# Kernel tuning notes

Measured on AMD Instinct MI355X. Metric: run time of the kernel, lower is better.

## Reference

```python
import jax, jax.numpy as jnp
import numpy as np

B, N, K, E, H, V = 128, 256, 4, 300, 150, 32000  # batch, nodes/tree, max children, embed, hidden, vocab
DELTA = 1.0


def setup_inputs() -> dict:
    key = jax.random.key(0)
    ks = jax.random.split(key, 8)
    query = jax.random.randint(ks[0], (B, N), 0, V, dtype=jnp.int32)
    pos = jax.random.randint(ks[1], (B, N), 0, V, dtype=jnp.int32)
    neg = jax.random.randint(ks[2], (B, N), 0, V, dtype=jnp.int32)
    # Complete K-ary tree over N nodes: children of node t are {K*t+1, ..., K*t+K} < N; root = node 0.
    ch = np.full((N, K), -1, dtype=np.int32)
    for t in range(N):
        for j in range(K):
            c = K * t + 1 + j
            if c < N:
                ch[t, j] = c
    children = jnp.asarray(ch)
    emb = jax.random.normal(ks[3], (V, E), dtype=jnp.float32) * 0.02
    W_iou = jax.random.normal(ks[4], (E, 3 * H), dtype=jnp.float32) * 0.05
    U_iou = jax.random.normal(ks[5], (H, 3 * H), dtype=jnp.float32) * 0.05
    b_iou = jnp.zeros((3 * H,), jnp.float32)
    W_f = jax.random.normal(ks[6], (E, H), dtype=jnp.float32) * 0.05
    U_f = jax.random.normal(ks[7], (H, H), dtype=jnp.float32) * 0.05
    b_f = jnp.zeros((H,), jnp.float32)
    return {"query": query, "pos": pos, "neg": neg, "children": children,
            "emb": emb, "W_iou": W_iou, "U_iou": U_iou, "b_iou": b_iou,
            "W_f": W_f, "U_f": U_f, "b_f": b_f}


def _childsum_treelstm(x, children, W_iou, U_iou, b_iou, W_f, U_f, b_f):
    """x: [B, N, E] node embeddings. Returns root (c, h): each [B, H]."""
    Bn, Nn, _ = x.shape
    Hh = U_f.shape[0]
    h0 = jnp.zeros((Bn, Nn, Hh), x.dtype)
    c0 = jnp.zeros((Bn, Nn, Hh), x.dtype)

    def step(carry, t):
        h_all, c_all = carry
        ch = children[t]                        # [K] child indices, -1 = padding
        mask = (ch >= 0)
        idx = jnp.where(mask, ch, 0)
        m = mask.astype(x.dtype)[None, :, None]  # [1, K, 1]
        h_k = h_all[:, idx] * m                 # [B, K, H]
        c_k = c_all[:, idx] * m
        h_sum = h_k.sum(axis=1)                 # child-sum h_tilde [B, H]
        x_t = x[:, t]                           # [B, E]
        iou = x_t @ W_iou + h_sum @ U_iou + b_iou
        i, o, u = jnp.split(iou, 3, axis=-1)
        i = jax.nn.sigmoid(i)
        o = jax.nn.sigmoid(o)
        u = jnp.tanh(u)
        # per-child forget gates: f_jk = sigmoid(W_f x_j + U_f h_k + b_f)
        f = jax.nn.sigmoid((x_t @ W_f + b_f)[:, None, :] + h_k @ U_f)  # [B, K, H]
        c_t = i * u + (f * c_k).sum(axis=1)     # c_k already masked
        h_t = o * jnp.tanh(c_t)
        return (h_all.at[:, t].set(h_t), c_all.at[:, t].set(c_t)), None

    # children have larger indices than parents -> process N-1 .. 0 (root last)
    (h_all, c_all), _ = jax.lax.scan(step, (h0, c0), jnp.arange(Nn - 1, -1, -1))
    return c_all[:, 0], h_all[:, 0]


def _cosine(a, b):
    num = (a * b).sum(-1)
    den = jnp.sqrt((a * a).sum(-1) * (b * b).sum(-1)) + 1e-8
    return num / den


def reference(query, pos, neg, children, emb, W_iou, U_iou, b_iou, W_f, U_f, b_f):
    qc, _ = _childsum_treelstm(emb[query], children, W_iou, U_iou, b_iou, W_f, U_f, b_f)
    pc, _ = _childsum_treelstm(emb[pos], children, W_iou, U_iou, b_iou, W_f, U_f, b_f)
    nc, _ = _childsum_treelstm(emb[neg], children, W_iou, U_iou, b_iou, W_f, U_f, b_f)
    a = _cosine(qc, pc)  # [B]
    b = _cosine(qc, nc)  # [B]
    return jax.nn.relu(DELTA - a + b)
```

## Files before the change

### kernel.cpp

```cpp
#include <hip/hip_runtime.h>
#include <hip/hip_bf16.h>

typedef short short8 __attribute__((ext_vector_type(8)));
typedef float floatx4 __attribute__((ext_vector_type(4)));
typedef unsigned short ushort;

#define Bb 128
#define Nn 256
#define Hh 150
#define HK 160
#define Vv 32000
#define NROW 384
#define PROJC 600
#define NINT 64
#define ZROW (Vv + NROW * NINT)

#define WTN 640

__device__ __forceinline__ float sigf(float x) { return 1.0f / (1.0f + __expf(-x)); }
__device__ __forceinline__ float tanhf_(float x) { return 1.0f - 2.0f / (__expf(2.0f * x) + 1.0f); }
__device__ __forceinline__ float bf2f(ushort s) { union { float f; unsigned u; } v; v.u = ((unsigned)s) << 16; return v.f; }
__device__ __forceinline__ ushort f2bf(float f) { __hip_bfloat16 h = __float2bfloat16(f); return *(ushort*)&h; }

__global__ __launch_bounds__(256) void k_prep(
    const float* __restrict__ W_iou, const float* __restrict__ W_f,
    const float* __restrict__ U_iou, const float* __restrict__ U_f,
    const float* __restrict__ b_iou, const float* __restrict__ b_f,
    short* __restrict__ Wt, short* __restrict__ Uti, short* __restrict__ Utf,
    float* __restrict__ biasw, ushort* __restrict__ h_u, float* __restrict__ c_u)
{
    int idx = blockIdx.x * 256 + threadIdx.x;
    const int nWt = 320 * WTN, nUi = 160 * 464, nUf = 160 * 160;
    if (idx < nWt) {
        int k = idx / WTN, n = idx % WTN;
        float v = 0.f;
        if (k < 300) { if (n < 450) v = W_iou[k * 450 + n]; else if (n < 600) v = W_f[k * 150 + (n - 450)]; }
        Wt[n * 320 + k] = (short)f2bf(v);
    } else if (idx < nWt + nUi) {
        int i2 = idx - nWt; int k = i2 / 464, n = i2 % 464;
        float v = (k < 150 && n < 450) ? U_iou[k * 450 + n] : 0.f;
        Uti[n * 160 + k] = (short)f2bf(v);
    } else if (idx < nWt + nUi + nUf) {
        int i2 = idx - nWt - nUi; int k = i2 / 160, n = i2 % 160;
        float v = (k < 150 && n < 150) ? U_f[k * 150 + n] : 0.f;
        Utf[n * 160 + k] = (short)f2bf(v);
    } else if (idx < nWt + nUi + nUf + WTN) {
        int n = idx - nWt - nUi - nUf;
        biasw[n] = n < 450 ? b_iou[n] : (n < 600 ? b_f[n - 450] : 0.f);
    } else if (idx < nWt + nUi + nUf + WTN + HK) {
        int k = idx - (nWt + nUi + nUf + WTN);
        h_u[(long)ZROW * HK + k] = 0;
        c_u[(long)ZROW * HK + k] = 0.f;
    }
}

__global__ __launch_bounds__(256) void k_vproj(
    const float* __restrict__ emb, const short* __restrict__ Wt,
    const float* __restrict__ biasw, ushort* __restrict__ proj)
{
    __shared__ __align__(16) short As[2][32][328];
    const int tid = threadIdx.x;

    const int bid = blockIdx.x;
    const int xcd = bid & 7, li = bid >> 3;
    const int wgid = xcd * 125 + li;

    const int cg = wgid % 5;
    const int rg = wgid / 5;
    const int rowbase = rg * 160;

    const int w = tid >> 6, lane = tid & 63;
    const int m = lane & 15, kq = (lane >> 4) * 8;
    const int t0 = cg * 8 + w * 2;
    const int col0 = t0 * 16 + m;
    const int col1 = col0 + 16;

    short8 bq0[10], bq1[10];
    #pragma unroll
    for (int ks = 0; ks < 10; ks++) {
        bq0[ks] = *(const short8*)(Wt + (long)col0 * 320 + kq + ks * 32);
        bq1[ks] = *(const short8*)(Wt + (long)col1 * 320 + kq + ks * 32);
    }
    const float bias0 = biasw[col0];
    const float bias1 = biasw[col1];

    for (int i = tid; i < 2 * 32 * 5; i += 256) {
        int bz = i / 160, r2 = (i % 160) / 5, kk = (i % 5) * 4;
        *(short4*)&As[bz][r2][300 + kk] = make_short4(0, 0, 0, 0);
    }

    {
        const float4* src = (const float4*)emb + (long)rowbase * 75;
        for (int i = tid; i < 2400; i += 256) {
            int r = i / 75, k0 = (i % 75) * 4;
            float4 x = src[i];
            short4 sv;
            sv.x = (short)f2bf(x.x); sv.y = (short)f2bf(x.y);
            sv.z = (short)f2bf(x.z); sv.w = (short)f2bf(x.w);
            *(short4*)&As[0][r][k0] = sv;
        }
    }
    __syncthreads();

    for (int c = 0; c < 5; c++) {
        const int buf = c & 1;

        float4 x[10];
        if (c < 4) {
            const float4* src = (const float4*)emb + (long)(rowbase + (c + 1) * 32) * 75;
            #pragma unroll
            for (int j = 0; j < 10; j++) {
                int i = tid + j * 256;
                if (i < 2400) x[j] = src[i];
            }
        }

        floatx4 a00 = {0.f,0.f,0.f,0.f}, a01 = a00, a10 = a00, a11 = a00;
        #pragma unroll
        for (int ks = 0; ks < 10; ks++) {
            short8 a0 = *(const short8*)&As[buf][m][kq + ks * 32];
            short8 a1 = *(const short8*)&As[buf][16 + m][kq + ks * 32];
            a00 = __builtin_amdgcn_mfma_f32_16x16x32_bf16(a0, bq0[ks], a00, 0, 0, 0);
            a01 = __builtin_amdgcn_mfma_f32_16x16x32_bf16(a0, bq1[ks], a01, 0, 0, 0);
            a10 = __builtin_amdgcn_mfma_f32_16x16x32_bf16(a1, bq0[ks], a10, 0, 0, 0);
            a11 = __builtin_amdgcn_mfma_f32_16x16x32_bf16(a1, bq1[ks], a11, 0, 0, 0);
        }

        {
            int v0 = rowbase + c * 32;
            int rb = (lane >> 4) * 4;
            if (col0 < PROJC) {
                #pragma unroll
                for (int reg = 0; reg < 4; reg++) {
                    proj[(long)(v0 + rb + reg) * PROJC + col0]      = f2bf(a00[reg] + bias0);
                    proj[(long)(v0 + 16 + rb + reg) * PROJC + col0] = f2bf(a10[reg] + bias0);
                }
            }
            if (col1 < PROJC) {
                #pragma unroll
                for (int reg = 0; reg < 4; reg++) {
                    proj[(long)(v0 + rb + reg) * PROJC + col1]      = f2bf(a01[reg] + bias1);
                    proj[(long)(v0 + 16 + rb + reg) * PROJC + col1] = f2bf(a11[reg] + bias1);
                }
            }
        }

        if (c < 4) {
            #pragma unroll
            for (int j = 0; j < 10; j++) {
                int i = tid + j * 256;
                if (i < 2400) {
                    int r = i / 75, k0 = (i % 75) * 4;
                    short4 sv;
                    sv.x = (short)f2bf(x[j].x); sv.y = (short)f2bf(x[j].y);
                    sv.z = (short)f2bf(x[j].z); sv.w = (short)f2bf(x[j].w);
                    *(short4*)&As[buf ^ 1][r][k0] = sv;
                }
            }
        }
        __syncthreads();
    }
}

__global__ __launch_bounds__(256) void k_vleaf(
    const ushort* __restrict__ proj, ushort* __restrict__ h_u, float* __restrict__ c_u)
{
    int idx = blockIdx.x * 256 + threadIdx.x;
    int v = idx / 20, k0 = (idx % 20) * 8;
    const ushort* pr = proj + (long)v * PROJC;
    ushort hv[8]; float cvv[8];
    #pragma unroll
    for (int e = 0; e < 8; e++) {
        int k = k0 + e;
        if (k < Hh) {
            float iv = sigf(bf2f(pr[k]));
            float ov = sigf(bf2f(pr[150 + k]));
            float uv = tanhf_(bf2f(pr[300 + k]));
            float cc = iv * uv;
            cvv[e] = cc;
            hv[e] = f2bf(ov * tanhf_(cc));
        } else { cvv[e] = 0.f; hv[e] = 0; }
    }
    *(int4*)(h_u + (long)v * HK + k0) = *(int4*)hv;
    *(float4*)(c_u + (long)v * HK + k0)     = make_float4(cvv[0], cvv[1], cvv[2], cvv[3]);
    *(float4*)(c_u + (long)v * HK + k0 + 4) = make_float4(cvv[4], cvv[5], cvv[6], cvv[7]);
}

__global__ __launch_bounds__(256) void k_level(
    int t_base, int t_cnt,
    const int* __restrict__ tq, const int* __restrict__ tp, const int* __restrict__ tn,
    const int* __restrict__ children, const ushort* __restrict__ proj,
    const short* __restrict__ Uti, const short* __restrict__ Utf,
    ushort* __restrict__ h_u, float* __restrict__ c_u)
{
    __shared__ __align__(16) short As[2][5][16][168];
    __shared__ int idx_s[2][16][4];
    __shared__ int tok_s[2][16];

    const int tid = threadIdx.x;
    const int chunk = blockIdx.x / 24;
    const int r0 = (blockIdx.x % 24) * 16;
    const int tA = t_base + chunk * 2;
    const int nT = min(2, t_base + t_cnt - tA);

    if (tid < 64 * nT) {
        int tt = tid >> 6, q = tid & 63;
        int r = q >> 2, j = q & 3;
        int t = tA + tt;
        int rg = r0 + r, g = rg >> 7, b = rg & 127;
        const int* tok = (g == 0) ? tq : (g == 1 ? tp : tn);
        int ch = children[t * 4 + j];
        int idx;
        if (ch < 0)        idx = ZROW;
        else if (ch >= 64) idx = tok[b * Nn + ch];
        else               idx = Vv + rg * NINT + ch;
        idx_s[tt][r][j] = idx;
        if (j == 0) tok_s[tt][r] = tok[b * Nn + t];
    }
    __syncthreads();

    for (int i = tid; i < 320 * nT; i += 256) {
        int tt = i / 320, i2 = i % 320;
        int r = i2 / 20, k0 = (i2 % 20) * 8;
        int4 v0 = *(const int4*)(h_u + (long)idx_s[tt][r][0] * HK + k0);
        int4 v1 = *(const int4*)(h_u + (long)idx_s[tt][r][1] * HK + k0);
        int4 v2 = *(const int4*)(h_u + (long)idx_s[tt][r][2] * HK + k0);
        int4 v3 = *(const int4*)(h_u + (long)idx_s[tt][r][3] * HK + k0);
        *(int4*)&As[tt][1][r][k0] = v0;
        *(int4*)&As[tt][2][r][k0] = v1;
        *(int4*)&As[tt][3][r][k0] = v2;
        *(int4*)&As[tt][4][r][k0] = v3;
        ushort s[8];
        const ushort* p0 = (const ushort*)&v0; const ushort* p1 = (const ushort*)&v1;
        const ushort* p2 = (const ushort*)&v2; const ushort* p3 = (const ushort*)&v3;
        #pragma unroll
        for (int e = 0; e < 8; e++)
            s[e] = f2bf(bf2f(p0[e]) + bf2f(p1[e]) + bf2f(p2[e]) + bf2f(p3[e]));
        *(int4*)&As[tt][0][r][k0] = *(int4*)s;
    }
    __syncthreads();

    const int w = tid >> 6, lane = tid & 63;
    const int m = lane & 15, kq = (lane >> 4) * 8;
    const int rbase = (lane >> 4) * 4;

    for (int nt = w; nt < 10; nt += 4) {
        int col = nt * 16 + m;

        short8 Bi[5], Bo[5], Bu[5], Bf[5];
        #pragma unroll
        for (int ks = 0; ks < 5; ks++) {
            Bi[ks] = *(const short8*)(Uti + (long)(col)       * HK + kq + ks * 32);
            Bo[ks] = *(const short8*)(Uti + (long)(150 + col) * HK + kq + ks * 32);
            Bu[ks] = *(const short8*)(Uti + (long)(300 + col) * HK + kq + ks * 32);
            Bf[ks] = *(const short8*)(Utf + (long)(col)       * HK + kq + ks * 32);
        }

        for (int tt = 0; tt < nT; ++tt) {
            int t = tA + tt;

            float pv0[4], pv1[4], pv2[4], pv3[4];
            float cu0[4], cu1[4], cu2[4], cu3[4];
            if (col < Hh) {
                #pragma unroll
                for (int reg = 0; reg < 4; reg++) {
                    const ushort* pr = proj + (long)tok_s[tt][rbase + reg] * PROJC;
                    pv0[reg] = bf2f(pr[col]);
                    pv1[reg] = bf2f(pr[150 + col]);
                    pv2[reg] = bf2f(pr[300 + col]);
                    pv3[reg] = bf2f(pr[450 + col]);
                    cu0[reg] = c_u[(long)idx_s[tt][rbase + reg][0] * HK + col];
                    cu1[reg] = c_u[(long)idx_s[tt][rbase + reg][1] * HK + col];
                    cu2[reg] = c_u[(long)idx_s[tt][rbase + reg][2] * HK + col];
                    cu3[reg] = c_u[(long)idx_s[tt][rbase + reg][3] * HK + col];
                }
            }

            floatx4 ai = {0.f,0.f,0.f,0.f}, ao = ai, au = ai;
            floatx4 af0 = ai, af1 = ai, af2 = ai, af3 = ai;
            #pragma unroll
            for (int ks = 0; ks < 5; ks++) {
                short8 asum = *(const short8*)&As[tt][0][m][kq + ks * 32];
                short8 ac0  = *(const short8*)&As[tt][1][m][kq + ks * 32];
                short8 ac1  = *(const short8*)&As[tt][2][m][kq + ks * 32];
                short8 ac2  = *(const short8*)&As[tt][3][m][kq + ks * 32];
                short8 ac3  = *(const short8*)&As[tt][4][m][kq + ks * 32];
                ai  = __builtin_amdgcn_mfma_f32_16x16x32_bf16(asum, Bi[ks], ai, 0, 0, 0);
                ao  = __builtin_amdgcn_mfma_f32_16x16x32_bf16(asum, Bo[ks], ao, 0, 0, 0);
                au  = __builtin_amdgcn_mfma_f32_16x16x32_bf16(asum, Bu[ks], au, 0, 0, 0);
                af0 = __builtin_amdgcn_mfma_f32_16x16x32_bf16(ac0,  Bf[ks], af0, 0, 0, 0);
                af1 = __builtin_amdgcn_mfma_f32_16x16x32_bf16(ac1,  Bf[ks], af1, 0, 0, 0);
                af2 = __builtin_amdgcn_mfma_f32_16x16x32_bf16(ac2,  Bf[ks], af2, 0, 0, 0);
                af3 = __builtin_amdgcn_mfma_f32_16x16x32_bf16(ac3,  Bf[ks], af3, 0, 0, 0);
            }

            if (col < Hh) {
                #pragma unroll
                for (int reg = 0; reg < 4; reg++) {
                    int rg = r0 + rbase + reg;
                    float iv = sigf(pv0[reg] + ai[reg]);
                    float ov = sigf(pv1[reg] + ao[reg]);
                    float uv = tanhf_(pv2[reg] + au[reg]);
                    float fpre = pv3[reg];
                    float cv = iv * uv;
                    cv = fmaf(sigf(fpre + af0[reg]), cu0[reg], cv);
                    cv = fmaf(sigf(fpre + af1[reg]), cu1[reg], cv);
                    cv = fmaf(sigf(fpre + af2[reg]), cu2[reg], cv);
                    cv = fmaf(sigf(fpre + af3[reg]), cu3[reg], cv);
                    long o = (long)(Vv + rg * NINT + t) * HK + col;
                    c_u[o] = cv;
                    h_u[o] = f2bf(ov * tanhf_(cv));
                }
            } else {
                #pragma unroll
                for (int reg = 0; reg < 4; reg++) {
                    long o = (long)(Vv + (r0 + rbase + reg) * NINT + t) * HK + col;
                    c_u[o] = 0.f; h_u[o] = 0;
                }
            }
        }
    }
}

__global__ __launch_bounds__(64) void k_cos(const float* __restrict__ c_u, float* __restrict__ out)
{
    int b = blockIdx.x, tid = threadIdx.x;
    const float* qc = c_u + (long)(Vv + (0 * Bb + b) * NINT) * HK;
    const float* pc = c_u + (long)(Vv + (1 * Bb + b) * NINT) * HK;
    const float* nc = c_u + (long)(Vv + (2 * Bb + b) * NINT) * HK;
    float qp = 0, qn = 0, qq = 0, pp = 0, nn2 = 0;
    for (int k = tid; k < Hh; k += 64) {
        float qv = qc[k], pv = pc[k], nv = nc[k];
        qp += qv * pv; qn += qv * nv; qq += qv * qv; pp += pv * pv; nn2 += nv * nv;
    }
    #pragma unroll
    for (int off = 32; off > 0; off >>= 1) {
        qp += __shfl_down(qp, off, 64);
        qn += __shfl_down(qn, off, 64);
        qq += __shfl_down(qq, off, 64);
        pp += __shfl_down(pp, off, 64);
        nn2 += __shfl_down(nn2, off, 64);
    }
    if (tid == 0) {
        float a = qp / (sqrtf(qq * pp) + 1e-8f);
        float d = qn / (sqrtf(qq * nn2) + 1e-8f);
        out[b] = fmaxf(0.0f, 1.0f - a + d);
    }
}

extern "C" void kernel_launch(void* const* d_in, const int* in_sizes, int n_in,
                              void* d_out, int out_size, void* d_ws, size_t ws_size,
                              hipStream_t stream)
{
    const int*   tq       = (const int*)d_in[0];
    const int*   tp       = (const int*)d_in[1];
    const int*   tn       = (const int*)d_in[2];
    const int*   children = (const int*)d_in[3];
    const float* emb      = (const float*)d_in[4];
    const float* W_iou    = (const float*)d_in[5];
    const float* U_iou    = (const float*)d_in[6];
    const float* b_iou    = (const float*)d_in[7];
    const float* W_f      = (const float*)d_in[8];
    const float* U_f      = (const float*)d_in[9];
    const float* b_f      = (const float*)d_in[10];
    float* out = (float*)d_out;

    char* ws = (char*)d_ws;
    ushort* proj  = (ushort*)ws;
    ushort* h_u   = (ushort*)(ws + 38400000);
    float*  c_u   = (float*)(ws + 56504640);
    short*  Wt    = (short*)(ws + 92713920);
    short*  Uti   = (short*)(ws + 93123520);
    short*  Utf   = (short*)(ws + 93272000);
    float*  biasw = (float*)(ws + 93323200);

    k_prep<<<1194, 256, 0, stream>>>(W_iou, W_f, U_iou, U_f, b_iou, b_f,
                                     Wt, Uti, Utf, biasw, h_u, c_u);
    k_vproj<<<1000, 256, 0, stream>>>(emb, Wt, biasw, proj);
    k_vleaf<<<2500, 256, 0, stream>>>(proj, h_u, c_u);
    k_level<<<22 * 24, 256, 0, stream>>>(21, 43, tq, tp, tn, children, proj, Uti, Utf, h_u, c_u);
    k_level<<<8 * 24, 256, 0, stream>>>(5, 16, tq, tp, tn, children, proj, Uti, Utf, h_u, c_u);
    k_level<<<2 * 24, 256, 0, stream>>>(1, 4,  tq, tp, tn, children, proj, Uti, Utf, h_u, c_u);
    k_level<<<1 * 24, 256, 0, stream>>>(0, 1,  tq, tp, tn, children, proj, Uti, Utf, h_u, c_u);
    k_cos<<<Bb, 64, 0, stream>>>(c_u, out);
}
```

Baseline: 249.7 us.

## Fuse last two tree levels into one kernel and double vproj rows per block

The final two level launches (nodes 1-4 and root) become a single kernel that runs three level steps in sequence with block barriers between them. This is valid because each block owns the same 16 rows across levels. The vocab projection kernel now has each workgroup process 320 rows over 10 chunks with half the blocks, giving a new XCD remap. Child and token indices in shared memory are narrowed to ushort. The fused kernel saves one launch and its tail, but the doubled vproj work per block lowers parallelism, and ushort indices could overflow for ZROW-range values.

```diff
diff --git a/kernel.cpp b/kernel.cpp
--- a/kernel.cpp
+++ b/kernel.cpp
@@ -63,11 +63,11 @@
 
     const int bid = blockIdx.x;
     const int xcd = bid & 7, li = bid >> 3;
-    const int wgid = xcd * 125 + li;
+    const int wgid = (xcd < 4 ? xcd * 63 : 252 + (xcd - 4) * 62) + li;
 
     const int cg = wgid % 5;
     const int rg = wgid / 5;
-    const int rowbase = rg * 160;
+    const int rowbase = rg * 320;
 
     const int w = tid >> 6, lane = tid & 63;
     const int m = lane & 15, kq = (lane >> 4) * 8;
@@ -102,11 +102,11 @@
     }
     __syncthreads();
 
-    for (int c = 0; c < 5; c++) {
+    for (int c = 0; c < 10; c++) {
         const int buf = c & 1;
 
         float4 x[10];
-        if (c < 4) {
+        if (c < 9) {
             const float4* src = (const float4*)emb + (long)(rowbase + (c + 1) * 32) * 75;
             #pragma unroll
             for (int j = 0; j < 10; j++) {
@@ -145,7 +145,7 @@
             }
         }
 
-        if (c < 4) {
+        if (c < 9) {
             #pragma unroll
             for (int j = 0; j < 10; j++) {
                 int i = tid + j * 256;
@@ -186,22 +186,16 @@
     *(float4*)(c_u + (long)v * HK + k0 + 4) = make_float4(cvv[4], cvv[5], cvv[6], cvv[7]);
 }
 
-__global__ __launch_bounds__(256) void k_level(
-    int t_base, int t_cnt,
+__device__ __forceinline__ void level_step(
+    int tA, int nT, int r0,
     const int* __restrict__ tq, const int* __restrict__ tp, const int* __restrict__ tn,
     const int* __restrict__ children, const ushort* __restrict__ proj,
     const short* __restrict__ Uti, const short* __restrict__ Utf,
-    ushort* __restrict__ h_u, float* __restrict__ c_u)
-{
-    __shared__ __align__(16) short As[2][5][16][168];
-    __shared__ int idx_s[2][16][4];
-    __shared__ int tok_s[2][16];
-
+    ushort* __restrict__ h_u, float* __restrict__ c_u,
+    short (*As)[16][168] ,
+    ushort (*idx_s)[16][4], ushort (*tok_s)[16])
+{
     const int tid = threadIdx.x;
-    const int chunk = blockIdx.x / 24;
-    const int r0 = (blockIdx.x % 24) * 16;
-    const int tA = t_base + chunk * 2;
-    const int nT = min(2, t_base + t_cnt - tA);
 
     if (tid < 64 * nT) {
         int tt = tid >> 6, q = tid & 63;
@@ -214,8 +208,8 @@
         if (ch < 0)        idx = ZROW;
         else if (ch >= 64) idx = tok[b * Nn + ch];
         else               idx = Vv + rg * NINT + ch;
-        idx_s[tt][r][j] = idx;
-        if (j == 0) tok_s[tt][r] = tok[b * Nn + t];
+        idx_s[tt][r][j] = (ushort)idx;
+        if (j == 0) tok_s[tt][r] = (ushort)tok[b * Nn + t];
     }
     __syncthreads();
 
@@ -226,17 +220,17 @@
         int4 v1 = *(const int4*)(h_u + (long)idx_s[tt][r][1] * HK + k0);
         int4 v2 = *(const int4*)(h_u + (long)idx_s[tt][r][2] * HK + k0);
         int4 v3 = *(const int4*)(h_u + (long)idx_s[tt][r][3] * HK + k0);
-        *(int4*)&As[tt][1][r][k0] = v0;
-        *(int4*)&As[tt][2][r][k0] = v1;
-        *(int4*)&As[tt][3][r][k0] = v2;
-        *(int4*)&As[tt][4][r][k0] = v3;
+        *(int4*)&As[tt * 5 + 1][r][k0] = v0;
+        *(int4*)&As[tt * 5 + 2][r][k0] = v1;
+        *(int4*)&As[tt * 5 + 3][r][k0] = v2;
+        *(int4*)&As[tt * 5 + 4][r][k0] = v3;
         ushort s[8];
         const ushort* p0 = (const ushort*)&v0; const ushort* p1 = (const ushort*)&v1;
         const ushort* p2 = (const ushort*)&v2; const ushort* p3 = (const ushort*)&v3;
         #pragma unroll
         for (int e = 0; e < 8; e++)
             s[e] = f2bf(bf2f(p0[e]) + bf2f(p1[e]) + bf2f(p2[e]) + bf2f(p3[e]));
-        *(int4*)&As[tt][0][r][k0] = *(int4*)s;
+        *(int4*)&As[tt * 5 + 0][r][k0] = *(int4*)s;
     }
     __syncthreads();
 
@@ -280,11 +274,11 @@
             floatx4 af0 = ai, af1 = ai, af2 = ai, af3 = ai;
             #pragma unroll
             for (int ks = 0; ks < 5; ks++) {
-                short8 asum = *(const short8*)&As[tt][0][m][kq + ks * 32];
-                short8 ac0  = *(const short8*)&As[tt][1][m][kq + ks * 32];
-                short8 ac1  = *(const short8*)&As[tt][2][m][kq + ks * 32];
-                short8 ac2  = *(const short8*)&As[tt][3][m][kq + ks * 32];
-                short8 ac3  = *(const short8*)&As[tt][4][m][kq + ks * 32];
+                short8 asum = *(const short8*)&As[tt * 5 + 0][m][kq + ks * 32];
+                short8 ac0  = *(const short8*)&As[tt * 5 + 1][m][kq + ks * 32];
+                short8 ac1  = *(const short8*)&As[tt * 5 + 2][m][kq + ks * 32];
+                short8 ac2  = *(const short8*)&As[tt * 5 + 3][m][kq + ks * 32];
+                short8 ac3  = *(const short8*)&As[tt * 5 + 4][m][kq + ks * 32];
                 ai  = __builtin_amdgcn_mfma_f32_16x16x32_bf16(asum, Bi[ks], ai, 0, 0, 0);
                 ao  = __builtin_amdgcn_mfma_f32_16x16x32_bf16(asum, Bo[ks], ao, 0, 0, 0);
                 au  = __builtin_amdgcn_mfma_f32_16x16x32_bf16(asum, Bu[ks], au, 0, 0, 0);
@@ -322,6 +316,48 @@
     }
 }
 
+__global__ __launch_bounds__(256) void k_level(
+    int t_base, int t_cnt,
+    const int* __restrict__ tq, const int* __restrict__ tp, const int* __restrict__ tn,
+    const int* __restrict__ children, const ushort* __restrict__ proj,
+    const short* __restrict__ Uti, const short* __restrict__ Utf,
+    ushort* __restrict__ h_u, float* __restrict__ c_u)
+{
+    __shared__ __align__(16) short As[10][16][168];
+    __shared__ ushort idx_s[2][16][4];
+    __shared__ ushort tok_s[2][16];
+
+    const int chunk = blockIdx.x / 24;
+    const int r0 = (blockIdx.x % 24) * 16;
+    const int tA = t_base + chunk * 2;
+    const int nT = min(2, t_base + t_cnt - tA);
+
+    level_step(tA, nT, r0, tq, tp, tn, children, proj, Uti, Utf, h_u, c_u,
+               As, idx_s, tok_s);
+}
+
+__global__ __launch_bounds__(256) void k_l34(
+    const int* __restrict__ tq, const int* __restrict__ tp, const int* __restrict__ tn,
+    const int* __restrict__ children, const ushort* __restrict__ proj,
+    const short* __restrict__ Uti, const short* __restrict__ Utf,
+    ushort* __restrict__ h_u, float* __restrict__ c_u)
+{
+    __shared__ __align__(16) short As[10][16][168];
+    __shared__ ushort idx_s[2][16][4];
+    __shared__ ushort tok_s[2][16];
+
+    const int r0 = blockIdx.x * 16;
+
+    level_step(1, 2, r0, tq, tp, tn, children, proj, Uti, Utf, h_u, c_u,
+               As, idx_s, tok_s);
+    __syncthreads();
+    level_step(3, 2, r0, tq, tp, tn, children, proj, Uti, Utf, h_u, c_u,
+               As, idx_s, tok_s);
+    __syncthreads();
+    level_step(0, 1, r0, tq, tp, tn, children, proj, Uti, Utf, h_u, c_u,
+               As, idx_s, tok_s);
+}
+
 __global__ __launch_bounds__(64) void k_cos(const float* __restrict__ c_u, float* __restrict__ out)
 {
     int b = blockIdx.x, tid = threadIdx.x;
@@ -376,11 +412,10 @@
 
     k_prep<<<1194, 256, 0, stream>>>(W_iou, W_f, U_iou, U_f, b_iou, b_f,
                                      Wt, Uti, Utf, biasw, h_u, c_u);
-    k_vproj<<<1000, 256, 0, stream>>>(emb, Wt, biasw, proj);
+    k_vproj<<<500, 256, 0, stream>>>(emb, Wt, biasw, proj);
     k_vleaf<<<2500, 256, 0, stream>>>(proj, h_u, c_u);
     k_level<<<22 * 24, 256, 0, stream>>>(21, 43, tq, tp, tn, children, proj, Uti, Utf, h_u, c_u);
     k_level<<<8 * 24, 256, 0, stream>>>(5, 16, tq, tp, tn, children, proj, Uti, Utf, h_u, c_u);
-    k_level<<<2 * 24, 256, 0, stream>>>(1, 4,  tq, tp, tn, children, proj, Uti, Utf, h_u, c_u);
-    k_level<<<1 * 24, 256, 0, stream>>>(0, 1,  tq, tp, tn, children, proj, Uti, Utf, h_u, c_u);
+    k_l34<<<24, 256, 0, stream>>>(tq, tp, tn, children, proj, Uti, Utf, h_u, c_u);
     k_cos<<<Bb, 64, 0, stream>>>(c_u, out);
 }
```

Measured after the change: 263.3 us. +5.5%, slower.
